# Performance work log

Measured on AMD Instinct MI355X. Metric: run time of the kernel, lower is better.

Reference implementation:

```python
import jax, jax.numpy as jnp
import numpy as np
import math

R = 3  # search_radius (init_kwargs)


def _normalize(x, eps=1e-6):
    # F.normalize(x, dim=1): x / max(||x||_2, eps)
    n = jnp.sqrt(jnp.sum(x * x, axis=1, keepdims=True))
    return x / jnp.maximum(n, eps)


def setup_inputs() -> dict:
    key = jax.random.key(0)
    k1, k2 = jax.random.split(key)
    B, D, H, W = 8, 64, 256, 256
    rubin_2d = jax.random.normal(k1, (B, D, H, W), dtype=jnp.float32)
    vis_2d = jax.random.normal(k2, (B, D, H, W), dtype=jnp.float32)
    log_temperature = jnp.asarray(math.log(0.1), dtype=jnp.float32)
    return {"rubin_2d": rubin_2d, "vis_2d": vis_2d, "log_temperature": log_temperature}


def reference(rubin_2d, vis_2d, log_temperature):
    B, D, H, W = rubin_2d.shape
    r = R
    K = (2 * r + 1) ** 2
    rubin_n = _normalize(rubin_2d)
    vis_n = _normalize(vis_2d)
    # replicate padding == 'edge'
    vis_pad = jnp.pad(vis_n, ((0, 0), (0, 0), (r, r), (r, r)), mode="edge")
    scale = 1.0 / math.sqrt(float(max(1, D)))
    # K=(2r+1)^2 shifted correlation maps (small fixed loop over displacements)
    corrs = []
    for dy in range(-r, r + 1):
        for dx in range(-r, r + 1):
            shifted = vis_pad[:, :, r + dy:r + dy + H, r + dx:r + dx + W]
            corrs.append(jnp.sum(rubin_n * shifted, axis=1) * scale)  # [B,H,W]
    logits = jnp.stack(corrs, axis=1)  # [B,K,H,W]

    offs = np.arange(-r, r + 1, dtype=np.float32)
    dy_lut = jnp.asarray(np.repeat(offs, 2 * r + 1)).reshape(1, K, 1, 1)
    dx_lut = jnp.asarray(np.tile(offs, 2 * r + 1)).reshape(1, K, 1, 1)

    tau = jnp.maximum(jnp.exp(log_temperature), 1e-3)
    probs_local = jax.nn.softmax(logits / tau, axis=1)  # [B,K,H,W]
    dy_local = jnp.sum(probs_local * dy_lut, axis=1, keepdims=True)
    dx_local = jnp.sum(probs_local * dx_lut, axis=1, keepdims=True)
    conf_local = jnp.max(probs_local, axis=1, keepdims=True)

    logits_global = jnp.mean(logits, axis=(2, 3), keepdims=True)  # [B,K,1,1]
    probs_global = jax.nn.softmax(logits_global / tau, axis=1)
    dy_global = jnp.sum(probs_global * dy_lut, axis=1, keepdims=True)
    dx_global = jnp.sum(probs_global * dx_lut, axis=1, keepdims=True)
    conf_global = jnp.max(probs_global, axis=1, keepdims=True)

    uniform = 1.0 / float(max(1, K))
    local_weight = jnp.clip((conf_local - uniform) / max(1e-6, 1.0 - uniform), 0.0, 1.0)
    dy = local_weight * dy_local + (1.0 - local_weight) * dy_global
    dx = local_weight * dx_local + (1.0 - local_weight) * dx_global
    return (dy, dx, conf_local, conf_global, local_weight, logits)
```

## Files before the change

kernel.cpp:

```cpp
#include <hip/hip_runtime.h>

#define HDIM 256
#define WDIM 256
#define DDIM 64
#define HWSZ (HDIM*WDIM)
#define NPIX 524288

#define TW 32
#define TH 16
#define BT 512
#define HW_T 38
#define HH_T 22
#define NPX 836
#define DC 8
#define NCH 8

typedef _Float16 f16;
typedef __attribute__((ext_vector_type(2))) _Float16 f16x2;

#if defined(__has_builtin)
# if __has_builtin(__builtin_amdgcn_fdot2)
#  define HAVE_FDOT2 1
# endif
#endif

__device__ __forceinline__ float fdot2(f16x2 a, f16x2 b, float c) {
#ifdef HAVE_FDOT2
    return __builtin_amdgcn_fdot2(a, b, c, false);
#else
    return c + (float)a.x * (float)b.x + (float)a.y * (float)b.y;
#endif
}

__device__ __forceinline__ float pk2(float a, float b) {
    f16x2 t; t.x = (f16)a; t.y = (f16)b;
    return __builtin_bit_cast(float, t);
}

__device__ __forceinline__ f16x2 bc(float x) {
    return __builtin_bit_cast(f16x2, x);
}

#define OFF_DY   0
#define OFF_DX   524288
#define OFF_CONF 1048576
#define OFF_CG   1572864
#define OFF_LW   1572872
#define OFF_LG   2097160

#define WS_GACC 0
#define WS_DYG  392
#define WS_DXG  400

__global__ void zero_ws_k(float* __restrict__ ws) {
    const int i = threadIdx.x;
    if (i < 408) ws[i] = 0.f;
}

__global__ void __launch_bounds__(BT, 4)
corr_main_k(const float* __restrict__ rub, const float* __restrict__ vis,
            const float* __restrict__ ltemp, float* __restrict__ out,
            float* __restrict__ ws)
{
    __shared__ __align__(16) float vis_s[NPX * 4];
    __shared__ float invv_s[NPX];
    __shared__ float gacc_s[49];

    const int tid = threadIdx.x;
    const int tx  = tid & 31;
    const int ty  = tid >> 5;
    const int w0  = blockIdx.x * TW;
    const int h0  = blockIdx.y * TH;
    const int b   = blockIdx.z;
    const int ibase = b * (DDIM * HWSZ);

    if (tid < 49) gacc_s[tid] = 0.f;

    const bool val1 = (tid + BT) < NPX;
    const int px1c  = val1 ? (tid + BT) : (NPX - 1);
    auto halo_goff = [&](int px) -> int {
        const int hr = px / HW_T;
        const int wc = px - hr * HW_T;
        const int gh = min(HDIM - 1, max(0, h0 - 3 + hr));
        const int gw = min(WDIM - 1, max(0, w0 - 3 + wc));
        return gh * WDIM + gw;
    };
    const int goff0 = halo_goff(tid);
    const int goff1 = halo_goff(px1c);
    const int pown  = (h0 + ty) * WDIM + (w0 + tx);
    const int l0 = tid * 4;
    const int l1 = px1c * 4;

    float acc[49];
#pragma unroll
    for (int k = 0; k < 49; ++k) acc[k] = 0.f;
    float sq0 = 0.f, sq1 = 0.f, sr = 0.f;

    float vv0[DC], vv1[DC], rn[DC];
#pragma unroll
    for (int d = 0; d < DC; ++d) {
        const int gof = ibase + d * HWSZ;
        vv0[d] = vis[gof + goff0];
        vv1[d] = vis[gof + goff1];
        rn[d]  = rub[gof + pown];
    }

    const float* vb = vis_s + (ty * HW_T + tx) * 4;
    f16x2 rh[4];

#pragma unroll 1
    for (int c = 0; c < NCH; ++c) {
        __syncthreads();
        *reinterpret_cast<float4*>(&vis_s[l0]) =
            make_float4(pk2(vv0[0], vv0[1]), pk2(vv0[2], vv0[3]),
                        pk2(vv0[4], vv0[5]), pk2(vv0[6], vv0[7]));
        *reinterpret_cast<float4*>(&vis_s[l1]) =
            make_float4(pk2(vv1[0], vv1[1]), pk2(vv1[2], vv1[3]),
                        pk2(vv1[4], vv1[5]), pk2(vv1[6], vv1[7]));
#pragma unroll
        for (int d = 0; d < DC; ++d) { sq0 += vv0[d] * vv0[d]; sq1 += vv1[d] * vv1[d]; }
#pragma unroll
        for (int j = 0; j < 4; ++j) { f16x2 t; t.x = (f16)rn[2*j]; t.y = (f16)rn[2*j+1]; rh[j] = t; }
#pragma unroll
        for (int d = 0; d < DC; ++d) sr += rn[d] * rn[d];
        __syncthreads();

        if (c < NCH - 1) {
#pragma unroll
            for (int d = 0; d < DC; ++d) {
                const int gof = ibase + ((c + 1) * DC + d) * HWSZ;
                vv0[d] = vis[gof + goff0];
                vv1[d] = vis[gof + goff1];
                rn[d]  = rub[gof + pown];
            }
        }

#pragma unroll
        for (int dyi = 0; dyi < 7; ++dyi) {
#pragma unroll
            for (int dxi = 0; dxi < 7; ++dxi) {
                const float4 v = *reinterpret_cast<const float4*>(
                    vb + (dyi * HW_T + dxi) * 4);
                float a = acc[dyi * 7 + dxi];
                a = fdot2(rh[0], bc(v.x), a);
                a = fdot2(rh[1], bc(v.y), a);
                a = fdot2(rh[2], bc(v.z), a);
                a = fdot2(rh[3], bc(v.w), a);
                acc[dyi * 7 + dxi] = a;
            }
        }
    }

    invv_s[tid] = 1.f / fmaxf(sqrtf(sq0), 1e-6f);
    if (val1) invv_s[tid + BT] = 1.f / fmaxf(sqrtf(sq1), 1e-6f);
    __syncthreads();

    const float tau  = fmaxf(__expf(ltemp[0]), 1e-3f);
    const float itau = 1.f / tau;
    const float invr = 1.f / fmaxf(sqrtf(sr), 1e-6f);
    const float cR   = invr * 0.125f;
    const float uu   = 1.f / 49.f;
    const float i1mu = 49.f / 48.f;

    const int h = h0 + ty, w = w0 + tx;
    const int lgbase = OFF_LG + b * 49 * HWSZ + h * WDIM + w;
    float mlg = -1e30f;
#pragma unroll
    for (int dyi = 0; dyi < 7; ++dyi) {
        const int rowb = (ty + dyi) * HW_T + tx;
#pragma unroll
        for (int dxi = 0; dxi < 7; ++dxi) {
            const int k = dyi * 7 + dxi;
            const float lg = acc[k] * cR * invv_s[rowb + dxi];
            out[lgbase + k * HWSZ] = lg;
            acc[k] = lg;
            mlg = fmaxf(mlg, lg);
        }
    }
    const float m = mlg * itau;
    float S = 0.f, sdy = 0.f, sdx = 0.f;
#pragma unroll
    for (int dyi = 0; dyi < 7; ++dyi) {
#pragma unroll
        for (int dxi = 0; dxi < 7; ++dxi) {
            const float e = __expf(fmaf(acc[dyi * 7 + dxi], itau, -m));
            S += e;
            sdy += e * (float)(dyi - 3);
            sdx += e * (float)(dxi - 3);
        }
    }
    const float invS = 1.f / S;
    const float conf = invS;
    const float lw   = fminf(fmaxf((conf - uu) * i1mu, 0.f), 1.f);
    const int po = b * HWSZ + h * WDIM + w;
    out[OFF_CONF + po] = conf;
    out[OFF_LW   + po] = lw;
    out[OFF_DY   + po] = sdy * invS;
    out[OFF_DX   + po] = sdx * invS;

#pragma unroll
    for (int k = 0; k < 49; ++k) {
        float v = acc[k];
#pragma unroll
        for (int off = 32; off > 0; off >>= 1)
            v += __shfl_xor(v, off, 64);
        if ((tid & 63) == 0) atomicAdd(&gacc_s[k], v);
    }
    __syncthreads();
    if (tid < 49) atomicAdd(&ws[WS_GACC + b * 49 + tid], gacc_s[tid]);
}

__global__ void glob_branch_k(const float* __restrict__ ltemp,
                              float* __restrict__ out, float* __restrict__ ws)
{
    const int t = threadIdx.x;
    if (t >= 8) return;
    const float tau  = fmaxf(__expf(ltemp[0]), 1e-3f);
    const float itau = 1.f / tau;
    float tk[49];
    float m = -1e30f;
#pragma unroll
    for (int k = 0; k < 49; ++k) {
        const float mean = ws[WS_GACC + t * 49 + k] * (1.f / 65536.f);
        tk[k] = mean * itau;
        m = fmaxf(m, tk[k]);
    }
    float S = 0.f, sdy = 0.f, sdx = 0.f;
#pragma unroll
    for (int k = 0; k < 49; ++k) {
        const float e = __expf(tk[k] - m);
        S += e;
        sdy += e * (float)(k / 7 - 3);
        sdx += e * (float)(k % 7 - 3);
    }
    const float invS = 1.f / S;
    out[OFF_CG + t] = invS;
    ws[WS_DYG + t] = sdy * invS;
    ws[WS_DXG + t] = sdx * invS;
}

__global__ void combine_k(float* __restrict__ out, const float* __restrict__ ws)
{
    const int gid = blockIdx.x * 256 + threadIdx.x;
    if (gid >= NPIX) return;
    const int b = gid >> 16;
    const float lw  = out[OFF_LW + gid];
    const float dyl = out[OFF_DY + gid];
    const float dxl = out[OFF_DX + gid];
    out[OFF_DY + gid] = lw * dyl + (1.f - lw) * ws[WS_DYG + b];
    out[OFF_DX + gid] = lw * dxl + (1.f - lw) * ws[WS_DXG + b];
}

extern "C" void kernel_launch(void* const* d_in, const int* in_sizes, int n_in,
                              void* d_out, int out_size, void* d_ws, size_t ws_size,
                              hipStream_t stream)
{
    const float* rub = (const float*)d_in[0];
    const float* vis = (const float*)d_in[1];
    const float* lt  = (const float*)d_in[2];
    float* out = (float*)d_out;
    float* ws  = (float*)d_ws;

    hipLaunchKernelGGL(zero_ws_k, dim3(1), dim3(512), 0, stream, ws);
    hipLaunchKernelGGL(corr_main_k, dim3(WDIM / TW, HDIM / TH, 8), dim3(BT), 0, stream,
                       rub, vis, lt, out, ws);
    hipLaunchKernelGGL(glob_branch_k, dim3(1), dim3(64), 0, stream, lt, out, ws);
    hipLaunchKernelGGL(combine_k, dim3(NPIX / 256), dim3(256), 0, stream, out, ws);
}
```

Measured before the change: 386.9 us.

## Give each wavefront a private halo tile to drop block-wide barriers

The block shrinks to 256 threads covering 8 rows. Each of the 4 wavefronts now stages its own 38x8 halo of vis (two output rows plus the radius-3 margin) in a private LDS region, so the per-chunk __syncthreads pairs go away and each wave relies on in-wavefront ordering. The cost is redundant halo loads across waves (8 rows per 2 output rows instead of 22 per 16) and 40 extra registers of prefetch state per thread, which may reduce occupancy. The final block reduction is also restructured to buffer the shuffled sums before the shared atomics.

Result: slower. 723.5 us (+87.0%).

```diff
diff --git a/kernel.cpp b/kernel.cpp
--- a/kernel.cpp
+++ b/kernel.cpp
@@ -7,11 +7,14 @@
 #define NPIX 524288
 
 #define TW 32
-#define TH 16
-#define BT 512
-#define HW_T 38
-#define HH_T 22
-#define NPX 836
+#define TH 8
+#define BT 256
+#define NW 4
+#define RR 38
+#define RH 8
+#define RPX 304
+#define NST 5
+#define RSTR 4
 #define DC 8
 #define NCH 8
 
@@ -62,77 +65,80 @@
             const float* __restrict__ ltemp, float* __restrict__ out,
             float* __restrict__ ws)
 {
-    __shared__ __align__(16) float vis_s[NPX * 4];
-    __shared__ float invv_s[NPX];
+    __shared__ __align__(16) float vis_s[NW * RPX * RSTR];
+    __shared__ float invv_s[NW * RPX];
     __shared__ float gacc_s[49];
 
-    const int tid = threadIdx.x;
-    const int tx  = tid & 31;
-    const int ty  = tid >> 5;
-    const int w0  = blockIdx.x * TW;
-    const int h0  = blockIdx.y * TH;
-    const int b   = blockIdx.z;
+    const int tid  = threadIdx.x;
+    const int wv   = tid >> 6;
+    const int lane = tid & 63;
+    const int hl   = lane >> 5;
+    const int tx   = lane & 31;
+    const int ty   = 2 * wv + hl;
+    const int w0 = blockIdx.x * TW;
+    const int h0 = blockIdx.y * TH;
+    const int b  = blockIdx.z;
     const int ibase = b * (DDIM * HWSZ);
 
     if (tid < 49) gacc_s[tid] = 0.f;
 
-    const bool val1 = (tid + BT) < NPX;
-    const int px1c  = val1 ? (tid + BT) : (NPX - 1);
-    auto halo_goff = [&](int px) -> int {
-        const int hr = px / HW_T;
-        const int wc = px - hr * HW_T;
-        const int gh = min(HDIM - 1, max(0, h0 - 3 + hr));
-        const int gw = min(WDIM - 1, max(0, w0 - 3 + wc));
-        return gh * WDIM + gw;
-    };
-    const int goff0 = halo_goff(tid);
-    const int goff1 = halo_goff(px1c);
-    const int pown  = (h0 + ty) * WDIM + (w0 + tx);
-    const int l0 = tid * 4;
-    const int l1 = px1c * 4;
+    int gso[NST], ivof[NST];
+#pragma unroll
+    for (int j = 0; j < NST; ++j) {
+        int p = lane + 64 * j; if (p > RPX - 1) p = RPX - 1;
+        const int row = p / RR;
+        const int col = p - row * RR;
+        const int gh = min(HDIM - 1, max(0, h0 + 2 * wv - 3 + row));
+        const int gw = min(WDIM - 1, max(0, w0 - 3 + col));
+        gso[j]  = gh * WDIM + gw;
+        ivof[j] = wv * RPX + p;
+    }
+    const int pown = (h0 + ty) * WDIM + (w0 + tx);
 
     float acc[49];
 #pragma unroll
     for (int k = 0; k < 49; ++k) acc[k] = 0.f;
-    float sq0 = 0.f, sq1 = 0.f, sr = 0.f;
-
-    float vv0[DC], vv1[DC], rn[DC];
-#pragma unroll
-    for (int d = 0; d < DC; ++d) {
-        const int gof = ibase + d * HWSZ;
-        vv0[d] = vis[gof + goff0];
-        vv1[d] = vis[gof + goff1];
-        rn[d]  = rub[gof + pown];
-    }
-
-    const float* vb = vis_s + (ty * HW_T + tx) * 4;
+    float sqa[NST] = {0.f, 0.f, 0.f, 0.f, 0.f};
+    float sr = 0.f;
+
+    float vv[NST][DC], rn[DC];
+#pragma unroll
+    for (int j = 0; j < NST; ++j)
+#pragma unroll
+        for (int d = 0; d < DC; ++d) vv[j][d] = vis[ibase + d * HWSZ + gso[j]];
+#pragma unroll
+    for (int d = 0; d < DC; ++d) rn[d] = rub[ibase + d * HWSZ + pown];
+
+    const float* vb = &vis_s[(wv * RPX + hl * RR + tx) * RSTR];
+    const float* ib = &invv_s[wv * RPX + hl * RR + tx];
     f16x2 rh[4];
 
 #pragma unroll 1
     for (int c = 0; c < NCH; ++c) {
-        __syncthreads();
-        *reinterpret_cast<float4*>(&vis_s[l0]) =
-            make_float4(pk2(vv0[0], vv0[1]), pk2(vv0[2], vv0[3]),
-                        pk2(vv0[4], vv0[5]), pk2(vv0[6], vv0[7]));
-        *reinterpret_cast<float4*>(&vis_s[l1]) =
-            make_float4(pk2(vv1[0], vv1[1]), pk2(vv1[2], vv1[3]),
-                        pk2(vv1[4], vv1[5]), pk2(vv1[6], vv1[7]));
-#pragma unroll
-        for (int d = 0; d < DC; ++d) { sq0 += vv0[d] * vv0[d]; sq1 += vv1[d] * vv1[d]; }
-#pragma unroll
-        for (int j = 0; j < 4; ++j) { f16x2 t; t.x = (f16)rn[2*j]; t.y = (f16)rn[2*j+1]; rh[j] = t; }
-#pragma unroll
-        for (int d = 0; d < DC; ++d) sr += rn[d] * rn[d];
-        __syncthreads();
-
-        if (c < NCH - 1) {
-#pragma unroll
-            for (int d = 0; d < DC; ++d) {
-                const int gof = ibase + ((c + 1) * DC + d) * HWSZ;
-                vv0[d] = vis[gof + goff0];
-                vv1[d] = vis[gof + goff1];
-                rn[d]  = rub[gof + pown];
-            }
+#pragma unroll
+        for (int j = 0; j < NST; ++j) {
+            *reinterpret_cast<float4*>(&vis_s[ivof[j] * RSTR]) =
+                make_float4(pk2(vv[j][0], vv[j][1]), pk2(vv[j][2], vv[j][3]),
+                            pk2(vv[j][4], vv[j][5]), pk2(vv[j][6], vv[j][7]));
+#pragma unroll
+            for (int d = 0; d < DC; ++d) sqa[j] = fmaf(vv[j][d], vv[j][d], sqa[j]);
+        }
+#pragma unroll
+        for (int jj = 0; jj < 4; ++jj) {
+            f16x2 t; t.x = (f16)rn[2*jj]; t.y = (f16)rn[2*jj+1]; rh[jj] = t;
+        }
+#pragma unroll
+        for (int d = 0; d < DC; ++d) sr = fmaf(rn[d], rn[d], sr);
+
+        if (c + 1 < NCH) {
+#pragma unroll
+            for (int j = 0; j < NST; ++j)
+#pragma unroll
+                for (int d = 0; d < DC; ++d)
+                    vv[j][d] = vis[ibase + ((c + 1) * DC + d) * HWSZ + gso[j]];
+#pragma unroll
+            for (int d = 0; d < DC; ++d)
+                rn[d] = rub[ibase + ((c + 1) * DC + d) * HWSZ + pown];
         }
 
 #pragma unroll
@@ -140,7 +146,7 @@
 #pragma unroll
             for (int dxi = 0; dxi < 7; ++dxi) {
                 const float4 v = *reinterpret_cast<const float4*>(
-                    vb + (dyi * HW_T + dxi) * 4);
+                    vb + (dyi * RR + dxi) * RSTR);
                 float a = acc[dyi * 7 + dxi];
                 a = fdot2(rh[0], bc(v.x), a);
                 a = fdot2(rh[1], bc(v.y), a);
@@ -151,9 +157,9 @@
         }
     }
 
-    invv_s[tid] = 1.f / fmaxf(sqrtf(sq0), 1e-6f);
-    if (val1) invv_s[tid + BT] = 1.f / fmaxf(sqrtf(sq1), 1e-6f);
-    __syncthreads();
+#pragma unroll
+    for (int j = 0; j < NST; ++j)
+        invv_s[ivof[j]] = 1.f / fmaxf(sqrtf(sqa[j]), 1e-6f);
 
     const float tau  = fmaxf(__expf(ltemp[0]), 1e-3f);
     const float itau = 1.f / tau;
@@ -167,11 +173,10 @@
     float mlg = -1e30f;
 #pragma unroll
     for (int dyi = 0; dyi < 7; ++dyi) {
-        const int rowb = (ty + dyi) * HW_T + tx;
 #pragma unroll
         for (int dxi = 0; dxi < 7; ++dxi) {
             const int k = dyi * 7 + dxi;
-            const float lg = acc[k] * cR * invv_s[rowb + dxi];
+            const float lg = acc[k] * cR * ib[dyi * RR + dxi];
             out[lgbase + k * HWSZ] = lg;
             acc[k] = lg;
             mlg = fmaxf(mlg, lg);
@@ -204,7 +209,12 @@
 #pragma unroll
         for (int off = 32; off > 0; off >>= 1)
             v += __shfl_xor(v, off, 64);
-        if ((tid & 63) == 0) atomicAdd(&gacc_s[k], v);
+        acc[k] = v;
+    }
+    __syncthreads();
+    if ((tid & 63) == 0) {
+#pragma unroll
+        for (int k = 0; k < 49; ++k) atomicAdd(&gacc_s[k], acc[k]);
     }
     __syncthreads();
     if (tid < 49) atomicAdd(&ws[WS_GACC + b * 49 + tid], gacc_s[tid]);
```
